# Kernel optimization log

Measured on AMD Instinct MI355X. Metric: run time of the kernel, lower is better.

The kernel has to match this reference:

```python
import jax, jax.numpy as jnp
import numpy as np

B, C, H, W = 8, 3, 64, 64
HORIZON = 32
WIDTH = 32
M1 = M2 = M3 = 8
N_LAYERS = 4
C_OUT = 3


def setup_inputs() -> dict:
    key = jax.random.key(0)
    ks = jax.random.split(key, 16)
    scale = 1.0 / (WIDTH * WIDTH)
    wshape = (N_LAYERS, 4, WIDTH, WIDTH, M1, M2, M3)
    return {
        "x_t": jax.random.normal(ks[0], (B, C, H, W), dtype=jnp.float32),
        "p_w": jax.random.normal(ks[1], (WIDTH, C + 3), dtype=jnp.float32) * 0.1,
        "p_b": jnp.zeros((WIDTH,), dtype=jnp.float32),
        "spec_wr": scale * jax.random.normal(ks[2], wshape, dtype=jnp.float32),
        "spec_wi": scale * jax.random.normal(ks[3], wshape, dtype=jnp.float32),
        "pw_w": jax.random.normal(ks[4], (N_LAYERS, WIDTH, WIDTH), dtype=jnp.float32) * 0.1,
        "pw_b": jnp.zeros((N_LAYERS, WIDTH), dtype=jnp.float32),
        "q1_w": jax.random.normal(ks[5], (2 * WIDTH, WIDTH), dtype=jnp.float32) * 0.1,
        "q1_b": jnp.zeros((2 * WIDTH,), dtype=jnp.float32),
        "q2_w": jax.random.normal(ks[6], (C_OUT, 2 * WIDTH), dtype=jnp.float32) * 0.1,
        "q2_b": jnp.zeros((C_OUT,), dtype=jnp.float32),
        "horizon": HORIZON,
    }


def _conv1x1(x, w, b):
    # x: [b, i, x, y, z], w: [o, i] -> [b, o, x, y, z]
    return jnp.einsum("oi,bixyz->boxyz", w, x) + b[None, :, None, None, None]


def _spectral_conv3d(x, wr, wi):
    # x: [b, i, H, W, T]; wr/wi: [4, i, o, m1, m2, m3]
    h, w_, t = x.shape[-3], x.shape[-2], x.shape[-1]
    xf = jnp.fft.rfftn(x, axes=(-3, -2, -1))  # [b, i, H, W, T//2+1]
    wc = (wr + 1j * wi).astype(xf.dtype)
    m1 = min(M1, xf.shape[-3]); m2 = min(M2, xf.shape[-2]); m3 = min(M3, xf.shape[-1])
    mul = lambda a, ww: jnp.einsum("bixyz,ioxyz->boxyz", a, ww)
    out = jnp.zeros((x.shape[0], wr.shape[2]) + xf.shape[2:], dtype=xf.dtype)
    out = out.at[:, :, :m1, :m2, :m3].set(mul(xf[:, :, :m1, :m2, :m3], wc[0, :, :, :m1, :m2, :m3]))
    out = out.at[:, :, -m1:, :m2, :m3].set(mul(xf[:, :, -m1:, :m2, :m3], wc[1, :, :, :m1, :m2, :m3]))
    out = out.at[:, :, :m1, -m2:, :m3].set(mul(xf[:, :, :m1, -m2:, :m3], wc[2, :, :, :m1, :m2, :m3]))
    out = out.at[:, :, -m1:, -m2:, :m3].set(mul(xf[:, :, -m1:, -m2:, :m3], wc[3, :, :, :m1, :m2, :m3]))
    return jnp.fft.irfftn(out, s=(h, w_, t), axes=(-3, -2, -1))


def _grid_3d(b, h, w, t, dtype):
    gy = jnp.broadcast_to(jnp.linspace(0.0, 1.0, h, dtype=dtype)[None, None, :, None, None], (b, 1, h, w, t))
    gx = jnp.broadcast_to(jnp.linspace(0.0, 1.0, w, dtype=dtype)[None, None, None, :, None], (b, 1, h, w, t))
    gt = jnp.broadcast_to(jnp.linspace(0.0, 1.0, t, dtype=dtype)[None, None, None, None, :], (b, 1, h, w, t))
    return jnp.concatenate([gy, gx, gt], axis=1)


def reference(x_t, p_w, p_b, spec_wr, spec_wi, pw_w, pw_b, q1_w, q1_b, q2_w, q2_b, horizon):
    b, c, h, w = x_t.shape
    x = jnp.broadcast_to(x_t[..., None], (b, c, h, w, horizon))  # repeat over time
    grid = _grid_3d(b, h, w, horizon, x_t.dtype)
    x = jnp.concatenate([x, grid], axis=1)  # [b, c+3, h, w, t]
    x = _conv1x1(x, p_w, p_b)
    for l in range(N_LAYERS):
        x = jax.nn.gelu(
            _spectral_conv3d(x, spec_wr[l], spec_wi[l]) + _conv1x1(x, pw_w[l], pw_b[l]),
            approximate=False,
        )
    x = _conv1x1(x, q1_w, q1_b)
    x = jax.nn.gelu(x, approximate=False)
    x = _conv1x1(x, q2_w, q2_b)
    # [b, c_out, h, w, t] -> [b, t, c_out, h, w]
    return jnp.transpose(x, (0, 4, 1, 2, 3))
```

## Files before the change

### kernel.cpp

```cpp
#include <hip/hip_runtime.h>
#include <math.h>


#define TWO_PI 6.2831853071795864769f

typedef short bf16x8 __attribute__((ext_vector_type(8)));
typedef float f32x4 __attribute__((ext_vector_type(4)));
typedef float v2f __attribute__((ext_vector_type(2)));

__device__ __forceinline__ f32x4 mfma16(bf16x8 a, bf16x8 b, f32x4 c) {
    return __builtin_amdgcn_mfma_f32_16x16x32_bf16(a, b, c, 0, 0, 0);
}

__device__ __forceinline__ void split8(float4 a, float4 b, bf16x8& h, bf16x8& l) {
    float f[8] = {a.x, a.y, a.z, a.w, b.x, b.y, b.z, b.w};
    #pragma unroll
    for (int i = 0; i < 8; ++i) {
        unsigned u = __float_as_uint(f[i]);
        h[i] = (short)(u >> 16);
        float hf = __uint_as_float(u & 0xFFFF0000u);
        float lf = f[i] - hf;
        l[i] = (short)(__float_as_uint(lf) >> 16);
    }
}

__device__ __forceinline__ v2f make2(float x) { v2f r; r.x = x; r.y = x; return r; }
__device__ __forceinline__ v2f fma2(v2f a, v2f b, v2f c) { return __builtin_elementwise_fma(a, b, c); }

__device__ __forceinline__ v2f gelu2(v2f v) {
    v2f u = v * 0.70710678118654752f;
    v2f a = __builtin_elementwise_abs(u);
    v2f den = fma2(a, make2(0.3275911f), make2(1.0f));
    v2f t; t.x = __builtin_amdgcn_rcpf(den.x); t.y = __builtin_amdgcn_rcpf(den.y);
    v2f p = t * (0.254829592f + t * (-0.284496736f + t * (1.421413741f +
            t * (-1.453152027f + t * 1.061405429f))));
    v2f e; e.x = __expf(-u.x * u.x); e.y = __expf(-u.y * u.y);
    v2f m = fma2(-p, e, make2(1.0f));
    v2f erfu = __builtin_elementwise_copysign(m, u);
    return 0.5f * v * (1.0f + erfu);
}

__device__ __forceinline__ void gelu4(f32x4& q) {
    v2f p0; p0.x = q[0]; p0.y = q[1];
    v2f p1; p1.x = q[2]; p1.y = q[3];
    p0 = gelu2(p0); p1 = gelu2(p1);
    q[0] = p0.x; q[1] = p0.y; q[2] = p1.x; q[3] = p1.y;
}

#define GOERTZEL_CONSTS \
    const float C2[8] = {2.0f, 1.9615705608f, 1.8477590650f, 1.6629392246f, \
                         1.4142135624f, 1.1111404660f, 0.7653668647f, 0.3901806440f}; \
    const float CK[8] = {1.0f, 0.9807852804f, 0.9238795325f, 0.8314696123f, \
                         0.7071067812f, 0.5555702330f, 0.3826834324f, 0.1950903220f}; \
    const float SK[8] = {0.0f, 0.1950903220f, 0.3826834324f, 0.5555702330f, \
                         0.7071067812f, 0.8314696123f, 0.9238795325f, 0.9807852804f};

#define GOERTZEL_EO(col, STRIDE, emit_ptr) { \
    GOERTZEL_CONSTS \
    float s1[8], s2[8]; \
    _Pragma("unroll") \
    for (int k = 0; k < 8; ++k) { s1[k] = 0.f; s2[k] = 0.f; } \
    for (int tt = 0; tt < 16; ++tt) { \
        float x0 = (col)[tt * (STRIDE)], x1 = (col)[(tt + 16) * (STRIDE)]; \
        float ev = x0 + x1, ov = x0 - x1; \
        _Pragma("unroll") \
        for (int k = 0; k < 8; ++k) { \
            float v = (k & 1) ? ov : ev; \
            float s0 = v + C2[k] * s1[k] - s2[k]; \
            s2[k] = s1[k]; s1[k] = s0; \
        } \
    } \
    _Pragma("unroll") \
    for (int k = 0; k < 8; ++k) { \
        float R = CK[k] * s1[k] - s2[k]; \
        float I = SK[k] * s1[k]; \
        if (k & 1) { R = -R; I = -I; } \
        (emit_ptr)[k] = make_float2(R, I); \
    } }

#define MAKE_TWIDDLES(t) \
    float ck2[8], sk2[8]; \
    float c1, s1v; __sincosf((t) * (TWO_PI / 32.0f), &s1v, &c1); \
    ck2[1] = 2.0f * c1; sk2[1] = 2.0f * s1v; \
    _Pragma("unroll") \
    for (int k = 2; k < 8; ++k) { \
        float nc = ck2[k-1] * c1 - sk2[k-1] * s1v; \
        float ns = sk2[k-1] * c1 + ck2[k-1] * s1v; \
        ck2[k] = nc; sk2[k] = ns; \
    }

__global__ __launch_bounds__(256) void k_lift(const float* __restrict__ xt,
                                              const float* __restrict__ pw,
                                              const float* __restrict__ pb,
                                              float* __restrict__ X,
                                              float2* __restrict__ T1) {
    __shared__ float xs[8448];
    int g = blockIdx.x;
    int spt = g & 511, b = g >> 9;
    int sp0 = spt * 8;
    int y = sp0 >> 6, x0 = sp0 & 63;
    int tid = threadIdx.x;
    int t = tid & 31, spl = tid >> 5;
    int sp = sp0 + spl;
    float a0 = xt[(b * 3 + 0) * 4096 + sp];
    float a1 = xt[(b * 3 + 1) * 4096 + sp];
    float a2 = xt[(b * 3 + 2) * 4096 + sp];
    float gy = y * (1.0f / 63.0f), gx = (x0 + spl) * (1.0f / 63.0f), gt = t * (1.0f / 31.0f);
    float v[32];
    #pragma unroll
    for (int c = 0; c < 32; ++c) {
        const float* w = pw + c * 6;
        v[c] = pb[c] + w[0] * a0 + w[1] * a1 + w[2] * a2
             + w[3] * gy + w[4] * gx + w[5] * gt;
    }
    float* xg = X + (((long)(b * 4096 + sp)) * 32 + t) * 32;
    #pragma unroll
    for (int j = 0; j < 8; ++j)
        ((float4*)xg)[j] = make_float4(v[4*j], v[4*j+1], v[4*j+2], v[4*j+3]);
    float* row = xs + (spl * 32 + t) * 33;
    #pragma unroll
    for (int c = 0; c < 32; ++c) row[c] = v[c];
    __syncthreads();
    int c = tid & 31, sl = tid >> 5;
    const float* col = xs + (sl * 32) * 33 + c;
    float2* ob = T1 + ((long)(b * 32 + c) * 4096 + sp0 + sl) * 8;
    GOERTZEL_EO(col, 33, ob)
}

__global__ __launch_bounds__(256) void k_xdft(const float2* __restrict__ T1, float2* __restrict__ T2) {
    __shared__ float2 s[1024];
    __shared__ float2 tw[64];
    int g = blockIdx.x;
    int ypair = g & 31; int bc = g >> 5;
    long base = ((long)bc * 64 + ypair * 2) * 512;
    int tid = threadIdx.x;
    for (int k = tid; k < 1024; k += 256) s[k] = T1[base + k];
    if (tid < 64) { float sn, cs; __sincosf(tid * (TWO_PI / 64.0f), &sn, &cs); tw[tid] = make_float2(cs, sn); }
    __syncthreads();
    #pragma unroll
    for (int r = 0; r < 2; ++r) {
        int j = tid + r * 256;
        int half = j >> 8, rem = j & 255;
        int idx = half * 512 + rem;
        float2 a = s[idx], b2 = s[idx + 256];
        s[idx] = make_float2(a.x + b2.x, a.y + b2.y);
        s[idx + 256] = make_float2(a.x - b2.x, a.y - b2.y);
    }
    __syncthreads();
    int half = tid >> 7, jj = tid & 127;
    int kxi = jj >> 3, kt = jj & 7;
    int kx = kxi < 8 ? kxi : kxi + 48;
    const float2* row = s + half * 512 + (kx & 1) * 256;
    float sr = 0.f, si = 0.f;
    for (int x = 0; x < 32; ++x) {
        float2 w = tw[(kx * x) & 63];
        float2 a = row[x * 8 + kt];
        sr += a.x * w.x + a.y * w.y;
        si += a.y * w.x - a.x * w.y;
    }
    T2[((long)bc * 64 + ypair * 2 + half) * 128 + jj] = make_float2(sr, si);
}

__global__ __launch_bounds__(128) void k_ydft(const float2* __restrict__ T2, float2* __restrict__ T3) {
    __shared__ float2 s[512];
    __shared__ float2 tw[64];
    int g = blockIdx.x;
    int kx = g & 15; int bc = g >> 4;
    int tid = threadIdx.x;
    for (int k = tid; k < 512; k += 128) {
        int y = k >> 3, kt = k & 7;
        s[k] = T2[((long)bc * 64 + y) * 128 + kx * 8 + kt];
    }
    if (tid < 64) { float sn, cs; __sincosf(tid * (TWO_PI / 64.0f), &sn, &cs); tw[tid] = make_float2(cs, sn); }
    __syncthreads();
    #pragma unroll
    for (int r = 0; r < 2; ++r) {
        int j = tid + r * 128;
        float2 a = s[j], b2 = s[j + 256];
        s[j] = make_float2(a.x + b2.x, a.y + b2.y);
        s[j + 256] = make_float2(a.x - b2.x, a.y - b2.y);
    }
    __syncthreads();
    int kyi = tid >> 3, kt = tid & 7;
    int ky = kyi < 8 ? kyi : kyi + 48;
    const float2* row = s + (ky & 1) * 256;
    float sr = 0.f, si = 0.f;
    for (int y = 0; y < 32; ++y) {
        float2 w = tw[(ky * y) & 63];
        float2 a = row[y * 8 + kt];
        sr += a.x * w.x + a.y * w.y;
        si += a.y * w.x - a.x * w.y;
    }
    T3[((long)bc * 256 + kyi * 16 + kx) * 8 + kt] = make_float2(sr, si);
}

__global__ __launch_bounds__(256) void k_mix2(const float2* __restrict__ T3,
                                              const float* __restrict__ wr,
                                              const float* __restrict__ wi,
                                              float2* __restrict__ T4, int layer) {
    __shared__ float2 s[2304];
    int mode = blockIdx.x;
    int kyi = mode >> 4, kxi = mode & 15;
    int tid = threadIdx.x;
    {
        int bb = tid >> 5, i = tid & 31;
        const float2* src = T3 + ((long)(bb * 32 + i) * 256 + mode) * 8;
        float2* dst = s + (i * 8 + bb) * 9;
        #pragma unroll
        for (int k = 0; k < 8; ++k) dst[k] = src[k];
    }
    __syncthreads();
    int corner = (kyi >= 8 ? 1 : 0) + (kxi >= 8 ? 2 : 0);
    long wbase = (long)(layer * 4 + corner) * 524288 + (long)(kyi & 7) * 64 + (long)(kxi & 7) * 8;
    int o = tid >> 3, kt = tid & 7;
    long wb = wbase + (long)o * 512 + kt;
    float2 acc[8];
    #pragma unroll
    for (int bb = 0; bb < 8; ++bb) acc[bb] = make_float2(0.f, 0.f);
    for (int i = 0; i < 32; ++i) {
        float r = wr[wb + (long)i * 16384], im = wi[wb + (long)i * 16384];
        #pragma unroll
        for (int bb = 0; bb < 8; ++bb) {
            float2 a = s[(i * 8 + bb) * 9 + kt];
            acc[bb].x += a.x * r - a.y * im;
            acc[bb].y += a.x * im + a.y * r;
        }
    }
    #pragma unroll
    for (int bb = 0; bb < 8; ++bb)
        T4[((long)(bb * 32 + o) * 256 + mode) * 8 + kt] = acc[bb];
}

__global__ __launch_bounds__(256) void k_invy(const float2* __restrict__ T4, float2* __restrict__ T5) {
    __shared__ float2 s[128];
    __shared__ float2 tw[64];
    __shared__ float2 pmP[56], pmM[56];
    int g = blockIdx.x;
    int kx = g & 15; int bc = g >> 4;
    int tid = threadIdx.x;
    if (tid < 128) {
        int kyi = tid >> 3, kt = tid & 7;
        s[tid] = T4[((long)bc * 256 + kyi * 16 + kx) * 8 + kt];
    } else if (tid < 192) {
        int m = tid - 128; float sn, cs; __sincosf(m * (TWO_PI / 64.0f), &sn, &cs); tw[m] = make_float2(cs, sn);
    }
    __syncthreads();
    if (tid < 56) {
        int j = (tid >> 3) + 1, kt = tid & 7;
        float2 a = s[j * 8 + kt], b2 = s[(16 - j) * 8 + kt];
        pmP[tid] = make_float2(a.x + b2.x, a.y + b2.y);
        pmM[tid] = make_float2(a.x - b2.x, a.y - b2.y);
    }
    __syncthreads();
    #pragma unroll
    for (int r = 0; r < 2; ++r) {
        int j = tid + r * 256;
        int y = j >> 3, kt = j & 7;
        float2 A0 = s[kt], A8 = s[64 + kt];
        float2 w8 = tw[(8 * y) & 63];
        float sr = A0.x + A8.x * w8.x + A8.y * w8.y;
        float si = A0.y + A8.y * w8.x - A8.x * w8.y;
        #pragma unroll
        for (int jj = 1; jj < 8; ++jj) {
            float2 w = tw[(jj * y) & 63];
            float2 P = pmP[(jj - 1) * 8 + kt], M = pmM[(jj - 1) * 8 + kt];
            sr += P.x * w.x - M.y * w.y;
            si += P.y * w.x + M.x * w.y;
        }
        T5[((long)bc * 64 + y) * 128 + kx * 8 + kt] = make_float2(sr, si);
    }
}

__global__ __launch_bounds__(256) void k_invx(const float2* __restrict__ T5, float2* __restrict__ T6) {
    __shared__ float2 s[128];
    __shared__ float2 tw[64];
    __shared__ float2 pmP[56], pmM[56];
    int g = blockIdx.x;
    int tid = threadIdx.x;
    if (tid < 128) {
        s[tid] = T5[(long)g * 128 + tid];
    } else if (tid < 192) {
        int m = tid - 128; float sn, cs; __sincosf(m * (TWO_PI / 64.0f), &sn, &cs); tw[m] = make_float2(cs, sn);
    }
    __syncthreads();
    if (tid < 56) {
        int j = (tid >> 3) + 1, kt = tid & 7;
        float2 a = s[j * 8 + kt], b2 = s[(16 - j) * 8 + kt];
        pmP[tid] = make_float2(a.x + b2.x, a.y + b2.y);
        pmM[tid] = make_float2(a.x - b2.x, a.y - b2.y);
    }
    __syncthreads();
    #pragma unroll
    for (int r = 0; r < 2; ++r) {
        int j = tid + r * 256;
        int x = j >> 3, kt = j & 7;
        float2 A0 = s[kt], A8 = s[64 + kt];
        float2 w8 = tw[(8 * x) & 63];
        float sr = A0.x + A8.x * w8.x + A8.y * w8.y;
        float si = A0.y + A8.y * w8.x - A8.x * w8.y;
        #pragma unroll
        for (int jj = 1; jj < 8; ++jj) {
            float2 w = tw[(jj * x) & 63];
            float2 P = pmP[(jj - 1) * 8 + kt], M = pmM[(jj - 1) * 8 + kt];
            sr += P.x * w.x - M.y * w.y;
            si += P.y * w.x + M.x * w.y;
        }
        T6[(long)g * 512 + j] = make_float2(sr, si);
    }
}

__global__ __launch_bounds__(256) void k_fuse3(float* __restrict__ X, const float2* __restrict__ T6,
                                               const float* __restrict__ pww,
                                               const float* __restrict__ pwb,
                                               float2* __restrict__ T1, int layer) {
    __shared__ float smem[9216];
    float2* ts = (float2*)smem;
    int g = blockIdx.x;
    int spt = g & 511, b = g >> 9;
    int sp0 = spt * 8;
    int tid = threadIdx.x;
    {
        int o = tid >> 3, spl = tid & 7;
        const float4* src = (const float4*)(T6 + ((long)(b * 32 + o) * 4096 + sp0 + spl) * 8);
        float4* dst = (float4*)(ts + o * 66 + spl * 8);
        const float S = 1.0f / 131072.0f;
        #pragma unroll
        for (int j = 0; j < 4; ++j) {
            float4 q = src[j];
            dst[j] = make_float4(q.x * S, q.y * S, q.z * S, q.w * S);
        }
    }
    int wave = tid >> 6, lane = tid & 63, l15 = lane & 15, quad = lane >> 4;
    int wb = wave * 64;
    const float* wl = pww + layer * 1024;
    const float* bl = pwb + layer * 32;
    bf16x8 wah[2], wal[2];
    f32x4 acc[2][4];
    #pragma unroll
    for (int mt = 0; mt < 2; ++mt) {
        const float4* p = (const float4*)(wl + (mt * 16 + l15) * 32 + quad * 8);
        split8(p[0], p[1], wah[mt], wal[mt]);
        float4 bv = *(const float4*)(bl + mt * 16 + quad * 4);
        f32x4 bi; bi[0] = bv.x; bi[1] = bv.y; bi[2] = bv.z; bi[3] = bv.w;
        #pragma unroll
        for (int nt = 0; nt < 4; ++nt) acc[mt][nt] = bi;
    }
    #pragma unroll
    for (int nt = 0; nt < 4; ++nt) {
        int pt = wb + nt * 16 + l15;
        int spl = pt >> 5, t = pt & 31;
        const float4* xp = (const float4*)(X + (((long)(b * 4096 + sp0 + spl)) * 32 + t) * 32 + quad * 8);
        bf16x8 bh, blo; split8(xp[0], xp[1], bh, blo);
        #pragma unroll
        for (int mt = 0; mt < 2; ++mt) {
            acc[mt][nt] = mfma16(wah[mt], bh, acc[mt][nt]);
            acc[mt][nt] = mfma16(wal[mt], bh, acc[mt][nt]);
            acc[mt][nt] = mfma16(wah[mt], blo, acc[mt][nt]);
        }
    }
    __syncthreads();
    MAKE_TWIDDLES(l15)
    #pragma unroll
    for (int mt = 0; mt < 2; ++mt)
        #pragma unroll
        for (int reg = 0; reg < 4; ++reg) {
            int o = mt * 16 + quad * 4 + reg;
            #pragma unroll
            for (int sph = 0; sph < 2; ++sph) {
                const float4* f4 = (const float4*)(ts + o * 66 + (2 * wave + sph) * 8);
                float4 q0 = f4[0], q1f = f4[1], q2f = f4[2], q3f = f4[3];
                float E = q0.x + q1f.x * ck2[2] - q1f.y * sk2[2]
                        + q2f.x * ck2[4] - q2f.y * sk2[4]
                        + q3f.x * ck2[6] - q3f.y * sk2[6];
                float O = q0.z * ck2[1] - q0.w * sk2[1]
                        + q1f.z * ck2[3] - q1f.w * sk2[3]
                        + q2f.z * ck2[5] - q2f.w * sk2[5]
                        + q3f.z * ck2[7] - q3f.w * sk2[7];
                acc[mt][sph * 2 + 0][reg] += E + O;
                acc[mt][sph * 2 + 1][reg] += E - O;
            }
        }
    #pragma unroll
    for (int mt = 0; mt < 2; ++mt)
        #pragma unroll
        for (int nt = 0; nt < 4; ++nt) gelu4(acc[mt][nt]);
    __syncthreads();
    #pragma unroll
    for (int mt = 0; mt < 2; ++mt)
        #pragma unroll
        for (int nt = 0; nt < 4; ++nt) {
            int pt = wb + nt * 16 + l15;
            int spl = pt >> 5, t = pt & 31;
            int o0 = mt * 16 + quad * 4;
            float4 w4 = make_float4(acc[mt][nt][0], acc[mt][nt][1], acc[mt][nt][2], acc[mt][nt][3]);
            *(float4*)(X + (((long)(b * 4096 + sp0 + spl)) * 32 + t) * 32 + o0) = w4;
            *(float4*)(smem + (spl * 32 + t) * 36 + o0) = w4;
        }
    __syncthreads();
    int c = tid & 31, sl = tid >> 5;
    const float* col = smem + (sl * 32) * 36 + c;
    float2* ob = T1 + ((long)(b * 32 + c) * 4096 + sp0 + sl) * 8;
    GOERTZEL_EO(col, 36, ob)
}

__global__ __launch_bounds__(256) void k_fuse3_last(const float* __restrict__ X, const float2* __restrict__ T6,
                                                    const float* __restrict__ pww, const float* __restrict__ pwb,
                                                    const float* __restrict__ q1w, const float* __restrict__ q1b,
                                                    const float* __restrict__ q2w, const float* __restrict__ q2b,
                                                    float* __restrict__ out) {
    __shared__ float smem[9408];
    float2* ts = (float2*)smem;
    int g = blockIdx.x;
    int spt = g & 511, b = g >> 9;
    int sp0 = spt * 8;
    int tid = threadIdx.x;
    {
        int o = tid >> 3, spl = tid & 7;
        const float4* src = (const float4*)(T6 + ((long)(b * 32 + o) * 4096 + sp0 + spl) * 8);
        float4* dst = (float4*)(ts + o * 66 + spl * 8);
        const float S = 1.0f / 131072.0f;
        #pragma unroll
        for (int j = 0; j < 4; ++j) {
            float4 q = src[j];
            dst[j] = make_float4(q.x * S, q.y * S, q.z * S, q.w * S);
        }
    }
    if (tid < 192) smem[9216 + tid] = q2w[tid];
    int wave = tid >> 6, lane = tid & 63, l15 = lane & 15, quad = lane >> 4;
    int wb = wave * 64;
    const float* wl = pww + 3 * 1024;
    const float* bl = pwb + 3 * 32;
    bf16x8 wah[2], wal[2];
    f32x4 acc[2][4];
    #pragma unroll
    for (int mt = 0; mt < 2; ++mt) {
        const float4* p = (const float4*)(wl + (mt * 16 + l15) * 32 + quad * 8);
        split8(p[0], p[1], wah[mt], wal[mt]);
        float4 bv = *(const float4*)(bl + mt * 16 + quad * 4);
        f32x4 bi; bi[0] = bv.x; bi[1] = bv.y; bi[2] = bv.z; bi[3] = bv.w;
        #pragma unroll
        for (int nt = 0; nt < 4; ++nt) acc[mt][nt] = bi;
    }
    #pragma unroll
    for (int nt = 0; nt < 4; ++nt) {
        int pt = wb + nt * 16 + l15;
        int spl = pt >> 5, t = pt & 31;
        const float4* xp = (const float4*)(X + (((long)(b * 4096 + sp0 + spl)) * 32 + t) * 32 + quad * 8);
        bf16x8 bh, blo; split8(xp[0], xp[1], bh, blo);
        #pragma unroll
        for (int mt = 0; mt < 2; ++mt) {
            acc[mt][nt] = mfma16(wah[mt], bh, acc[mt][nt]);
            acc[mt][nt] = mfma16(wal[mt], bh, acc[mt][nt]);
            acc[mt][nt] = mfma16(wah[mt], blo, acc[mt][nt]);
        }
    }
    __syncthreads();
    MAKE_TWIDDLES(l15)
    #pragma unroll
    for (int mt = 0; mt < 2; ++mt)
        #pragma unroll
        for (int reg = 0; reg < 4; ++reg) {
            int o = mt * 16 + quad * 4 + reg;
            #pragma unroll
            for (int sph = 0; sph < 2; ++sph) {
                const float4* f4 = (const float4*)(ts + o * 66 + (2 * wave + sph) * 8);
                float4 q0 = f4[0], q1f = f4[1], q2f = f4[2], q3f = f4[3];
                float E = q0.x + q1f.x * ck2[2] - q1f.y * sk2[2]
                        + q2f.x * ck2[4] - q2f.y * sk2[4]
                        + q3f.x * ck2[6] - q3f.y * sk2[6];
                float O = q0.z * ck2[1] - q0.w * sk2[1]
                        + q1f.z * ck2[3] - q1f.w * sk2[3]
                        + q2f.z * ck2[5] - q2f.w * sk2[5]
                        + q3f.z * ck2[7] - q3f.w * sk2[7];
                acc[mt][sph * 2 + 0][reg] += E + O;
                acc[mt][sph * 2 + 1][reg] += E - O;
            }
        }
    #pragma unroll
    for (int mt = 0; mt < 2; ++mt)
        #pragma unroll
        for (int nt = 0; nt < 4; ++nt) gelu4(acc[mt][nt]);
    __syncthreads();
    #pragma unroll
    for (int mt = 0; mt < 2; ++mt)
        #pragma unroll
        for (int nt = 0; nt < 4; ++nt) {
            int pt = wb + nt * 16 + l15;
            int o0 = mt * 16 + quad * 4;
            *(float4*)(smem + pt * 36 + o0) =
                make_float4(acc[mt][nt][0], acc[mt][nt][1], acc[mt][nt][2], acc[mt][nt][3]);
        }
    __syncthreads();
    bf16x8 qah[4], qal[4];
    f32x4 qbv[4];
    #pragma unroll
    for (int mt = 0; mt < 4; ++mt) {
        const float4* p = (const float4*)(q1w + (mt * 16 + l15) * 32 + quad * 8);
        split8(p[0], p[1], qah[mt], qal[mt]);
        float4 bv = *(const float4*)(q1b + mt * 16 + quad * 4);
        qbv[mt][0] = bv.x; qbv[mt][1] = bv.y; qbv[mt][2] = bv.z; qbv[mt][3] = bv.w;
    }
    const float* q2l = smem + 9216;
    float q2b0 = q2b[0], q2b1 = q2b[1], q2b2 = q2b[2];
    float oc0[4], oc1[4], oc2[4];
    #pragma unroll
    for (int nt = 0; nt < 4; ++nt) {
        int pt = wb + nt * 16 + l15;
        const float4* bp = (const float4*)(smem + pt * 36 + quad * 8);
        bf16x8 bh, blo; split8(bp[0], bp[1], bh, blo);
        float p0 = 0.f, p1 = 0.f, p2 = 0.f;
        #pragma unroll
        for (int mt = 0; mt < 4; ++mt) {
            f32x4 h = qbv[mt];
            h = mfma16(qah[mt], bh, h);
            h = mfma16(qal[mt], bh, h);
            h = mfma16(qah[mt], blo, h);
            gelu4(h);
            #pragma unroll
            for (int reg = 0; reg < 4; ++reg) {
                int hh = mt * 16 + quad * 4 + reg;
                p0 += q2l[hh] * h[reg];
                p1 += q2l[64 + hh] * h[reg];
                p2 += q2l[128 + hh] * h[reg];
            }
        }
        p0 += __shfl_xor(p0, 16); p0 += __shfl_xor(p0, 32);
        p1 += __shfl_xor(p1, 16); p1 += __shfl_xor(p1, 32);
        p2 += __shfl_xor(p2, 16); p2 += __shfl_xor(p2, 32);
        oc0[nt] = p0 + q2b0; oc1[nt] = p1 + q2b1; oc2[nt] = p2 + q2b2;
    }
    __syncthreads();
    if (quad == 0) {
        #pragma unroll
        for (int nt = 0; nt < 4; ++nt) {
            int pt = wb + nt * 16 + l15;
            int spl = pt >> 5, t = pt & 31;
            smem[(t * 3 + 0) * 9 + spl] = oc0[nt];
            smem[(t * 3 + 1) * 9 + spl] = oc1[nt];
            smem[(t * 3 + 2) * 9 + spl] = oc2[nt];
        }
    }
    __syncthreads();
    for (int m = tid; m < 768; m += 256) {
        int u = m >> 3, spl = m & 7;
        out[((long)(b * 96 + u)) * 4096 + sp0 + spl] = smem[u * 9 + spl];
    }
}

extern "C" void kernel_launch(void* const* d_in, const int* in_sizes, int n_in,
                              void* d_out, int out_size, void* d_ws, size_t ws_size,
                              hipStream_t stream) {
    const float* xt  = (const float*)d_in[0];
    const float* pw  = (const float*)d_in[1];
    const float* pb  = (const float*)d_in[2];
    const float* swr = (const float*)d_in[3];
    const float* swi = (const float*)d_in[4];
    const float* pww = (const float*)d_in[5];
    const float* pwb = (const float*)d_in[6];
    const float* q1w = (const float*)d_in[7];
    const float* q1b = (const float*)d_in[8];
    const float* q2w = (const float*)d_in[9];
    const float* q2b = (const float*)d_in[10];
    float* out = (float*)d_out;

    float*  X  = (float*)d_ws;
    float2* T1 = (float2*)(X + 33554432);
    float2* T2 = (float2*)((float*)T1 + 16777216);
    float2* T3 = (float2*)((float*)T2 + 4194304);
    float2* T4 = (float2*)((float*)T3 + 1048576);

    k_lift<<<4096, 256, 0, stream>>>(xt, pw, pb, X, T1);
    for (int l = 0; l < 4; ++l) {
        k_xdft<<<8192, 256, 0, stream>>>(T1, T2);
        k_ydft<<<4096, 128, 0, stream>>>(T2, T3);
        k_mix2<<<256, 256, 0, stream>>>(T3, swr, swi, T4, l);
        k_invy<<<4096, 256, 0, stream>>>(T4, T2);
        k_invx<<<16384, 256, 0, stream>>>(T2, T1);
        if (l < 3)
            k_fuse3<<<4096, 256, 0, stream>>>(X, T1, pww, pwb, T1, l);
        else
            k_fuse3_last<<<4096, 256, 0, stream>>>(X, T1, pww, pwb, q1w, q1b, q2w, q2b, out);
    }
}
```

Baseline: 830.6 us.

## Compute inverse time DFT with bf16x3 MFMA instead of scalar twiddle sums

Replaces the per-thread scalar inverse real DFT over the time axis (8 retained modes to 32 time points) in the fused layer kernels with a small matrix product on the MFMA units. The twiddle matrix is built in split-bf16 hi/lo form, and the spectral data is split the same way. Three MFMAs per tile keep the result close to fp32. The results go through shared memory and are added to the pointwise accumulators before GELU. This trades scalar FMAs for extra LDS round trips and two extra barriers, and half the lanes carry zero padding in the K dimension.

```diff
diff --git a/kernel.cpp b/kernel.cpp
--- a/kernel.cpp
+++ b/kernel.cpp
@@ -78,17 +78,6 @@
         (emit_ptr)[k] = make_float2(R, I); \
     } }
 
-#define MAKE_TWIDDLES(t) \
-    float ck2[8], sk2[8]; \
-    float c1, s1v; __sincosf((t) * (TWO_PI / 32.0f), &s1v, &c1); \
-    ck2[1] = 2.0f * c1; sk2[1] = 2.0f * s1v; \
-    _Pragma("unroll") \
-    for (int k = 2; k < 8; ++k) { \
-        float nc = ck2[k-1] * c1 - sk2[k-1] * s1v; \
-        float ns = sk2[k-1] * c1 + ck2[k-1] * s1v; \
-        ck2[k] = nc; sk2[k] = ns; \
-    }
-
 __global__ __launch_bounds__(256) void k_lift(const float* __restrict__ xt,
                                               const float* __restrict__ pw,
                                               const float* __restrict__ pb,
@@ -309,6 +298,30 @@
     }
 }
 
+__device__ __forceinline__ void make_invt_A(int l15, int quad, bf16x8 Ah[2], bf16x8 Al[2]) {
+    #pragma unroll
+    for (int th = 0; th < 2; ++th) {
+        float m[8];
+        if (quad < 2) {
+            int tt = th * 16 + l15;
+            #pragma unroll
+            for (int kk = 0; kk < 4; ++kk) {
+                int k = quad * 4 + kk;
+                float sn, cs;
+                __sincosf((float)(k * tt) * (TWO_PI / 32.0f), &sn, &cs);
+                float w = k ? 2.0f : 1.0f;
+                m[2 * kk] = w * cs;
+                m[2 * kk + 1] = -w * sn;
+            }
+        } else {
+            #pragma unroll
+            for (int j = 0; j < 8; ++j) m[j] = 0.f;
+        }
+        split8(make_float4(m[0], m[1], m[2], m[3]),
+               make_float4(m[4], m[5], m[6], m[7]), Ah[th], Al[th]);
+    }
+}
+
 __global__ __launch_bounds__(256) void k_fuse3(float* __restrict__ X, const float2* __restrict__ T6,
                                                const float* __restrict__ pww,
                                                const float* __restrict__ pwb,
@@ -358,33 +371,54 @@
             acc[mt][nt] = mfma16(wah[mt], blo, acc[mt][nt]);
         }
     }
-    __syncthreads();
-    MAKE_TWIDDLES(l15)
+    bf16x8 Ah[2], Al[2];
+    make_invt_A(l15, quad, Ah, Al);
+    __syncthreads();
+    bf16x8 Bh[2][2], Bl[2][2];
+    #pragma unroll
+    for (int sph = 0; sph < 2; ++sph) {
+        int spl = 2 * wave + sph;
+        #pragma unroll
+        for (int ch = 0; ch < 2; ++ch) {
+            float4 q0 = make_float4(0.f, 0.f, 0.f, 0.f), q1 = q0;
+            if (quad < 2) {
+                const float4* p = (const float4*)(ts + (ch * 16 + l15) * 66 + spl * 8 + quad * 4);
+                q0 = p[0]; q1 = p[1];
+            }
+            split8(q0, q1, Bh[sph][ch], Bl[sph][ch]);
+        }
+    }
+    __syncthreads();
+    #pragma unroll
+    for (int sph = 0; sph < 2; ++sph) {
+        int spl = 2 * wave + sph;
+        #pragma unroll
+        for (int ch = 0; ch < 2; ++ch)
+            #pragma unroll
+            for (int th = 0; th < 2; ++th) {
+                f32x4 d = {0.f, 0.f, 0.f, 0.f};
+                d = mfma16(Ah[th], Bh[sph][ch], d);
+                d = mfma16(Al[th], Bh[sph][ch], d);
+                d = mfma16(Ah[th], Bl[sph][ch], d);
+                float* wp = smem + (spl * 32 + th * 16 + quad * 4) * 36 + ch * 16 + l15;
+                wp[0] = d[0]; wp[36] = d[1]; wp[72] = d[2]; wp[108] = d[3];
+            }
+    }
+    __syncthreads();
     #pragma unroll
     for (int mt = 0; mt < 2; ++mt)
         #pragma unroll
-        for (int reg = 0; reg < 4; ++reg) {
-            int o = mt * 16 + quad * 4 + reg;
-            #pragma unroll
-            for (int sph = 0; sph < 2; ++sph) {
-                const float4* f4 = (const float4*)(ts + o * 66 + (2 * wave + sph) * 8);
-                float4 q0 = f4[0], q1f = f4[1], q2f = f4[2], q3f = f4[3];
-                float E = q0.x + q1f.x * ck2[2] - q1f.y * sk2[2]
-                        + q2f.x * ck2[4] - q2f.y * sk2[4]
-                        + q3f.x * ck2[6] - q3f.y * sk2[6];
-                float O = q0.z * ck2[1] - q0.w * sk2[1]
-                        + q1f.z * ck2[3] - q1f.w * sk2[3]
-                        + q2f.z * ck2[5] - q2f.w * sk2[5]
-                        + q3f.z * ck2[7] - q3f.w * sk2[7];
-                acc[mt][sph * 2 + 0][reg] += E + O;
-                acc[mt][sph * 2 + 1][reg] += E - O;
-            }
+        for (int nt = 0; nt < 4; ++nt) {
+            int pt = wb + nt * 16 + l15;
+            int spl = pt >> 5, t = pt & 31;
+            float4 sp4 = *(const float4*)(smem + (spl * 32 + t) * 36 + mt * 16 + quad * 4);
+            acc[mt][nt][0] += sp4.x; acc[mt][nt][1] += sp4.y;
+            acc[mt][nt][2] += sp4.z; acc[mt][nt][3] += sp4.w;
         }
     #pragma unroll
     for (int mt = 0; mt < 2; ++mt)
         #pragma unroll
         for (int nt = 0; nt < 4; ++nt) gelu4(acc[mt][nt]);
-    __syncthreads();
     #pragma unroll
     for (int mt = 0; mt < 2; ++mt)
         #pragma unroll
@@ -454,33 +488,54 @@
             acc[mt][nt] = mfma16(wah[mt], blo, acc[mt][nt]);
         }
     }
-    __syncthreads();
-    MAKE_TWIDDLES(l15)
+    bf16x8 Ah[2], Al[2];
+    make_invt_A(l15, quad, Ah, Al);
+    __syncthreads();
+    bf16x8 Bh[2][2], Bl[2][2];
+    #pragma unroll
+    for (int sph = 0; sph < 2; ++sph) {
+        int spl = 2 * wave + sph;
+        #pragma unroll
+        for (int ch = 0; ch < 2; ++ch) {
+            float4 q0 = make_float4(0.f, 0.f, 0.f, 0.f), q1 = q0;
+            if (quad < 2) {
+                const float4* p = (const float4*)(ts + (ch * 16 + l15) * 66 + spl * 8 + quad * 4);
+                q0 = p[0]; q1 = p[1];
+            }
+            split8(q0, q1, Bh[sph][ch], Bl[sph][ch]);
+        }
+    }
+    __syncthreads();
+    #pragma unroll
+    for (int sph = 0; sph < 2; ++sph) {
+        int spl = 2 * wave + sph;
+        #pragma unroll
+        for (int ch = 0; ch < 2; ++ch)
+            #pragma unroll
+            for (int th = 0; th < 2; ++th) {
+                f32x4 d = {0.f, 0.f, 0.f, 0.f};
+                d = mfma16(Ah[th], Bh[sph][ch], d);
+                d = mfma16(Al[th], Bh[sph][ch], d);
+                d = mfma16(Ah[th], Bl[sph][ch], d);
+                float* wp = smem + (spl * 32 + th * 16 + quad * 4) * 36 + ch * 16 + l15;
+                wp[0] = d[0]; wp[36] = d[1]; wp[72] = d[2]; wp[108] = d[3];
+            }
+    }
+    __syncthreads();
     #pragma unroll
     for (int mt = 0; mt < 2; ++mt)
         #pragma unroll
-        for (int reg = 0; reg < 4; ++reg) {
-            int o = mt * 16 + quad * 4 + reg;
-            #pragma unroll
-            for (int sph = 0; sph < 2; ++sph) {
-                const float4* f4 = (const float4*)(ts + o * 66 + (2 * wave + sph) * 8);
-                float4 q0 = f4[0], q1f = f4[1], q2f = f4[2], q3f = f4[3];
-                float E = q0.x + q1f.x * ck2[2] - q1f.y * sk2[2]
-                        + q2f.x * ck2[4] - q2f.y * sk2[4]
-                        + q3f.x * ck2[6] - q3f.y * sk2[6];
-                float O = q0.z * ck2[1] - q0.w * sk2[1]
-                        + q1f.z * ck2[3] - q1f.w * sk2[3]
-                        + q2f.z * ck2[5] - q2f.w * sk2[5]
-                        + q3f.z * ck2[7] - q3f.w * sk2[7];
-                acc[mt][sph * 2 + 0][reg] += E + O;
-                acc[mt][sph * 2 + 1][reg] += E - O;
-            }
+        for (int nt = 0; nt < 4; ++nt) {
+            int pt = wb + nt * 16 + l15;
+            int spl = pt >> 5, t = pt & 31;
+            float4 sp4 = *(const float4*)(smem + (spl * 32 + t) * 36 + mt * 16 + quad * 4);
+            acc[mt][nt][0] += sp4.x; acc[mt][nt][1] += sp4.y;
+            acc[mt][nt][2] += sp4.z; acc[mt][nt][3] += sp4.w;
         }
     #pragma unroll
     for (int mt = 0; mt < 2; ++mt)
         #pragma unroll
         for (int nt = 0; nt < 4; ++nt) gelu4(acc[mt][nt]);
-    __syncthreads();
     #pragma unroll
     for (int mt = 0; mt < 2; ++mt)
         #pragma unroll
```

Measured after the change: 811.5 us. 1.02x faster.
